# Performance work log

Measured on AMD Instinct MI355X. Metric: run time of the kernel, lower is better.

Reference implementation:

```python
import jax, jax.numpy as jnp
import numpy as np

N = 100000
E = 800000
F_IN = 64
HID = 128


def setup_inputs() -> dict:
    key = jax.random.key(0)
    ks = jax.random.split(key, 10)
    x = jax.random.normal(ks[0], (N, F_IN), dtype=jnp.float32)
    edge_index = jax.random.randint(ks[1], (2, E), 0, N, dtype=jnp.int64)
    s = 0.05
    # PyG GraphConv: lin_rel (with bias) applied to aggregated neighbors, lin_root (no bias) to self
    return {
        "x": x,
        "edge_index": edge_index,
        "W1_rel": jax.random.normal(ks[2], (HID, F_IN), dtype=jnp.float32) * s,
        "b1": jnp.zeros((HID,), dtype=jnp.float32),
        "W1_root": jax.random.normal(ks[3], (HID, F_IN), dtype=jnp.float32) * s,
        "W2_rel": jax.random.normal(ks[4], (HID, HID), dtype=jnp.float32) * s,
        "b2": jnp.zeros((HID,), dtype=jnp.float32),
        "W2_root": jax.random.normal(ks[5], (HID, HID), dtype=jnp.float32) * s,
        "W_fc1": jax.random.normal(ks[6], (20, HID), dtype=jnp.float32) * s,
        "b_fc1": jnp.zeros((20,), dtype=jnp.float32),
        "W_fc2": jax.random.normal(ks[7], (1, 20), dtype=jnp.float32) * s,
        "b_fc2": jnp.zeros((1,), dtype=jnp.float32),
    }


def graph_conv(x, edge_index, W_rel, b_rel, W_root):
    # sum-aggregate source features onto destination nodes (PyG GraphConv, aggr='add')
    src, dst = edge_index[0], edge_index[1]
    agg = jax.ops.segment_sum(x[src], dst, num_segments=N)  # [N, F]
    return agg @ W_rel.T + b_rel + x @ W_root.T


def reference(x, edge_index, W1_rel, b1, W1_root, W2_rel, b2, W2_root,
              W_fc1, b_fc1, W_fc2, b_fc2):
    h = graph_conv(x, edge_index, W1_rel, b1, W1_root)
    h = jax.nn.elu(h)
    h = graph_conv(h, edge_index, W2_rel, b2, W2_root)
    h = jax.nn.relu(h @ W_fc1.T + b_fc1)
    out = h @ W_fc2.T + b_fc2  # [N, 1]
    return out
```

## Files before the change

### kernel.cpp

```cpp
#include <hip/hip_runtime.h>

#define N_NODES 100000
#define N_EDGES 800000
#define FIN 64
#define HID 128
#define NB1 391
#define SRCS_CAP (N_EDGES + 3 * N_NODES)

typedef unsigned short ushort_t;
typedef __attribute__((ext_vector_type(8))) short short8;
typedef __attribute__((ext_vector_type(16))) float fx16;
typedef __attribute__((ext_vector_type(4))) unsigned short us4;

__device__ inline ushort_t f2bf(float f) {
    unsigned u = __float_as_uint(f);
    u += 0x7fffu + ((u >> 16) & 1u);
    return (ushort_t)(u >> 16);
}
__device__ inline float bf2f(ushort_t h) { return __uint_as_float(((unsigned)h) << 16); }

__device__ inline void upadd(float* acc, uint4 A) {
    acc[0] += __uint_as_float(A.x << 16);
    acc[1] += __uint_as_float(A.x & 0xffff0000u);
    acc[2] += __uint_as_float(A.y << 16);
    acc[3] += __uint_as_float(A.y & 0xffff0000u);
    acc[4] += __uint_as_float(A.z << 16);
    acc[5] += __uint_as_float(A.z & 0xffff0000u);
    acc[6] += __uint_as_float(A.w << 16);
    acc[7] += __uint_as_float(A.w & 0xffff0000u);
}

__global__ void zero_int_kernel(int* __restrict__ deg, int* __restrict__ flag,
                                int* __restrict__ srcs) {
    int i = blockIdx.x * 256 + threadIdx.x;
    if (i < N_NODES) deg[i] = 0;
    if (i == 0) *flag = 0;
    for (int k = i; k < SRCS_CAP; k += NB1 * 256) srcs[k] = N_NODES;
}

__global__ void detect_kernel(const int* __restrict__ w, int* __restrict__ flag) {
    int i = blockIdx.x * 256 + threadIdx.x;
    if (i < 8192) {
        if (w[2 * i + 1] != 0) atomicOr(flag, 1);
    }
}

__global__ void hist_kernel(const int* __restrict__ w, const int* __restrict__ flag,
                            int* __restrict__ deg, int* __restrict__ rank) {
    int e = blockIdx.x * 256 + threadIdx.x;
    if (e >= N_EDGES) return;
    int is32 = *flag;
    int d = is32 ? w[N_EDGES + e] : w[2 * (N_EDGES + e)];
    rank[e] = atomicAdd(&deg[d], 1);
}

__global__ void scan1_kernel(const int* __restrict__ deg, int* __restrict__ off,
                             int* __restrict__ bsums) {
    __shared__ int s[256];
    int t = threadIdx.x;
    int i = blockIdx.x * 256 + t;
    int v = (i < N_NODES) ? ((deg[i] + 3) & ~3) : 0;
    s[t] = v;
    __syncthreads();
    for (int d = 1; d < 256; d <<= 1) {
        int w = (t >= d) ? s[t - d] : 0;
        __syncthreads();
        s[t] += w;
        __syncthreads();
    }
    if (i < N_NODES) off[i] = s[t] - v;
    if (t == 255) bsums[blockIdx.x] = s[255];
}

__global__ void scan2_kernel(int* __restrict__ bsums) {
    __shared__ int s[512];
    int t = threadIdx.x;
    int v = (t < NB1) ? bsums[t] : 0;
    s[t] = v;
    __syncthreads();
    for (int d = 1; d < 512; d <<= 1) {
        int w = (t >= d) ? s[t - d] : 0;
        __syncthreads();
        s[t] += w;
        __syncthreads();
    }
    if (t < NB1) bsums[t] = s[t] - v;
    if (t == NB1 - 1) bsums[NB1] = s[t];
}

__global__ void scan3_kernel(int* __restrict__ off, const int* __restrict__ bsums) {
    int i = blockIdx.x * 256 + threadIdx.x;
    if (i < N_NODES) off[i] = off[i] + bsums[blockIdx.x];
    if (i == 0) off[N_NODES] = bsums[NB1];
}

__global__ void scatter_kernel(const int* __restrict__ w, const int* __restrict__ flag,
                               const int* __restrict__ off, const int* __restrict__ rank,
                               int* __restrict__ srcs) {
    int e = blockIdx.x * 256 + threadIdx.x;
    if (e >= N_EDGES) return;
    int is32 = *flag;
    int s = is32 ? w[e] : w[2 * e];
    int d = is32 ? w[N_EDGES + e] : w[2 * (N_EDGES + e)];
    srcs[off[d] + rank[e]] = s;
}

__global__ void cvt_kernel(const float* __restrict__ x, ushort_t* __restrict__ xb,
                           const float* __restrict__ W1rel, const float* __restrict__ W1root,
                           const float* __restrict__ W2rel, const float* __restrict__ W2root,
                           ushort_t* __restrict__ Wb1, ushort_t* __restrict__ Wb2,
                           ushort_t* __restrict__ h1b) {
    int i = blockIdx.x * 256 + threadIdx.x;
    if (i < N_NODES * FIN / 4) {
        float4 v = ((const float4*)x)[i];
        us4 o = {f2bf(v.x), f2bf(v.y), f2bf(v.z), f2bf(v.w)};
        ((us4*)xb)[i] = o;
    }
    us4 z = {0, 0, 0, 0};
    if (i < 16) ((us4*)xb)[(size_t)N_NODES * 16 + i] = z;
    if (i >= 16 && i < 48) ((us4*)h1b)[(size_t)N_NODES * 32 + (i - 16)] = z;
    if (i < HID * HID) {
        int n = i >> 7, k = i & 127;
        float v = (k < FIN) ? W1rel[n * FIN + k] : W1root[n * FIN + (k - FIN)];
        Wb1[i] = f2bf(v);
    }
    if (i < HID * 2 * HID) {
        int n = i >> 8, k = i & 255;
        float v = (k < HID) ? W2rel[n * HID + k] : W2root[n * HID + (k - HID)];
        Wb2[i] = f2bf(v);
    }
}

__global__ void agg1_kernel(const ushort_t* __restrict__ xb, const int* __restrict__ off,
                            const int* __restrict__ srcs, ushort_t* __restrict__ aggb) {
    int wid = (blockIdx.x * 256 + threadIdx.x) >> 6;
    int lane = threadIdx.x & 63;
    int n = lane >> 3;
    unsigned c = lane & 7;
    int node = wid * 8 + n;
    int b = off[node], e = off[node + 1];
    float acc[8];
#pragma unroll
    for (int j = 0; j < 8; j++) acc[j] = 0.f;
    const uint4* rows = (const uint4*)xb;
    for (int p = b; p < e; p += 4) {
        int4 s = *(const int4*)(srcs + p);
        uint4 A = rows[(unsigned)s.x * 8u + c];
        uint4 B = rows[(unsigned)s.y * 8u + c];
        uint4 C = rows[(unsigned)s.z * 8u + c];
        uint4 D = rows[(unsigned)s.w * 8u + c];
        upadd(acc, A);
        upadd(acc, B);
        upadd(acc, C);
        upadd(acc, D);
    }
    uint4 o = {(unsigned)f2bf(acc[0]) | ((unsigned)f2bf(acc[1]) << 16),
               (unsigned)f2bf(acc[2]) | ((unsigned)f2bf(acc[3]) << 16),
               (unsigned)f2bf(acc[4]) | ((unsigned)f2bf(acc[5]) << 16),
               (unsigned)f2bf(acc[6]) | ((unsigned)f2bf(acc[7]) << 16)};
    ((uint4*)(aggb + (size_t)node * FIN))[c] = o;
}

__global__ void agg2_kernel(const ushort_t* __restrict__ h1b, const int* __restrict__ off,
                            const int* __restrict__ srcs, ushort_t* __restrict__ aggb) {
    int wid = (blockIdx.x * 256 + threadIdx.x) >> 6;
    int lane = threadIdx.x & 63;
    int n = lane >> 4;
    unsigned c = lane & 15;
    int node = wid * 4 + n;
    int b = off[node], e = off[node + 1];
    float acc[8];
#pragma unroll
    for (int j = 0; j < 8; j++) acc[j] = 0.f;
    const uint4* rows = (const uint4*)h1b;
    for (int p = b; p < e; p += 4) {
        int4 s = *(const int4*)(srcs + p);
        uint4 A = rows[(unsigned)s.x * 16u + c];
        uint4 B = rows[(unsigned)s.y * 16u + c];
        uint4 C = rows[(unsigned)s.z * 16u + c];
        uint4 D = rows[(unsigned)s.w * 16u + c];
        upadd(acc, A);
        upadd(acc, B);
        upadd(acc, C);
        upadd(acc, D);
    }
    uint4 o = {(unsigned)f2bf(acc[0]) | ((unsigned)f2bf(acc[1]) << 16),
               (unsigned)f2bf(acc[2]) | ((unsigned)f2bf(acc[3]) << 16),
               (unsigned)f2bf(acc[4]) | ((unsigned)f2bf(acc[5]) << 16),
               (unsigned)f2bf(acc[6]) | ((unsigned)f2bf(acc[7]) << 16)};
    ((uint4*)(aggb + (size_t)node * HID))[c] = o;
}

__global__ __launch_bounds__(256) void g1_kernel(
    const ushort_t* __restrict__ aggb, const ushort_t* __restrict__ xb,
    const ushort_t* __restrict__ Wb1, const float* __restrict__ b1,
    ushort_t* __restrict__ h1b) {
    __shared__ short8 wl8[2048];
    ushort_t* wl = (ushort_t*)wl8;
#pragma unroll
    for (int it = 0; it < 8; it++) {
        int q = it * 256 + threadIdx.x;
        int n = q >> 4, c = q & 15;
        short8 v = ((const short8*)Wb1)[q];
        *(short8*)(wl + n * HID + ((c ^ (n & 7)) << 3)) = v;
    }
    __syncthreads();

    int wave = threadIdx.x >> 6;
    int lane = threadIdx.x & 63;
    int nb = blockIdx.x * 128 + wave * 32;
    if (nb >= N_NODES) return;
    int half = lane >> 5, col = lane & 31;
    int nA = nb + col;
    if (nA >= N_NODES) nA = N_NODES - 1;

    short8 areg[8];
#pragma unroll
    for (int s = 0; s < 4; s++)
        areg[s] = *(const short8*)(aggb + (size_t)nA * FIN + s * 16 + half * 8);
#pragma unroll
    for (int s = 4; s < 8; s++)
        areg[s] = *(const short8*)(xb + (size_t)nA * FIN + (s - 4) * 16 + half * 8);

    fx16 acc[4];
#pragma unroll
    for (int jt = 0; jt < 4; jt++)
#pragma unroll
        for (int r = 0; r < 16; r++) acc[jt][r] = 0.f;

#pragma unroll
    for (int s = 0; s < 8; s++) {
        int c = 2 * s + half;
#pragma unroll
        for (int jt = 0; jt < 4; jt++) {
            int n = jt * 32 + col;
            short8 bq = *(const short8*)(wl + n * HID + ((c ^ (n & 7)) << 3));
            acc[jt] = __builtin_amdgcn_mfma_f32_32x32x16_bf16(areg[s], bq, acc[jt], 0, 0, 0);
        }
    }
#pragma unroll
    for (int jt = 0; jt < 4; jt++) {
        int j = jt * 32 + col;
        float bias = b1[j];
#pragma unroll
        for (int r = 0; r < 16; r++) {
            int node = nb + (r & 3) + 8 * (r >> 2) + 4 * half;
            if (node < N_NODES) {
                float v = acc[jt][r] + bias;
                v = v > 0.f ? v : __expf(v) - 1.f;
                h1b[(size_t)node * HID + j] = f2bf(v);
            }
        }
    }
}

__global__ __launch_bounds__(256) void g2h_kernel(
    const ushort_t* __restrict__ agg2b, const ushort_t* __restrict__ h1b,
    const ushort_t* __restrict__ Wb2, const float* __restrict__ b2,
    const float* __restrict__ Wfc1, const float* __restrict__ bfc1,
    const float* __restrict__ Wfc2, const float* __restrict__ bfc2,
    float* __restrict__ out) {
    __shared__ ushort_t smem[21504];
    ushort_t* wl = smem;
    ushort_t* wf = smem + 17408;

#pragma unroll
    for (int it = 0; it < 16; it++) {
        int idx = it * 256 + threadIdx.x;
        int m = idx >> 7, k = idx & 127;
        float v = (m < 20) ? Wfc1[m * HID + k] : 0.f;
        wf[m * 128 + (((k >> 3) ^ (m & 7)) << 3) + (k & 7)] = f2bf(v);
    }
#pragma unroll
    for (int it = 0; it < 8; it++) {
        int q = it * 256 + threadIdx.x;
        int n = q >> 4, c = q & 15;
        short8 v = *(const short8*)(Wb2 + (size_t)n * 256 + c * 8);
        *(short8*)(wl + n * 128 + ((c ^ (n & 7)) << 3)) = v;
    }

    int wave = threadIdx.x >> 6;
    int lane = threadIdx.x & 63;
    int half = lane >> 5, col = lane & 31;
    int nb = blockIdx.x * 128 + wave * 32;
    int nA = nb + col;
    if (nA >= N_NODES) nA = N_NODES - 1;

    short8 areg[16];
#pragma unroll
    for (int s = 0; s < 8; s++)
        areg[s] = *(const short8*)(agg2b + (size_t)nA * HID + s * 16 + half * 8);
#pragma unroll
    for (int s = 8; s < 16; s++)
        areg[s] = *(const short8*)(h1b + (size_t)nA * HID + (s - 8) * 16 + half * 8);

    fx16 acc[4];
#pragma unroll
    for (int jt = 0; jt < 4; jt++)
#pragma unroll
        for (int r = 0; r < 16; r++) acc[jt][r] = 0.f;

    __syncthreads();
#pragma unroll
    for (int s = 0; s < 8; s++) {
        int c = 2 * s + half;
#pragma unroll
        for (int jt = 0; jt < 4; jt++) {
            int n = jt * 32 + col;
            short8 bq = *(const short8*)(wl + n * 128 + ((c ^ (n & 7)) << 3));
            acc[jt] = __builtin_amdgcn_mfma_f32_32x32x16_bf16(areg[s], bq, acc[jt], 0, 0, 0);
        }
    }
    __syncthreads();
#pragma unroll
    for (int it = 0; it < 8; it++) {
        int q = it * 256 + threadIdx.x;
        int n = q >> 4, c = q & 15;
        short8 v = *(const short8*)(Wb2 + (size_t)n * 256 + 128 + c * 8);
        *(short8*)(wl + n * 128 + ((c ^ (n & 7)) << 3)) = v;
    }
    __syncthreads();
#pragma unroll
    for (int s = 8; s < 16; s++) {
        int c = 2 * (s - 8) + half;
#pragma unroll
        for (int jt = 0; jt < 4; jt++) {
            int n = jt * 32 + col;
            short8 bq = *(const short8*)(wl + n * 128 + ((c ^ (n & 7)) << 3));
            acc[jt] = __builtin_amdgcn_mfma_f32_32x32x16_bf16(areg[s], bq, acc[jt], 0, 0, 0);
        }
    }
    __syncthreads();

    ushort_t* tl = smem;
#pragma unroll
    for (int jt = 0; jt < 4; jt++) {
        int j = jt * 32 + col;
        float bias = b2[j];
#pragma unroll
        for (int r = 0; r < 16; r++) {
            int nl = wave * 32 + (r & 3) + 8 * (r >> 2) + 4 * half;
            tl[nl * 136 + j] = f2bf(acc[jt][r] + bias);
        }
    }
    __syncthreads();

    short8 af[8];
#pragma unroll
    for (int s = 0; s < 8; s++)
        af[s] = *(const short8*)(tl + (wave * 32 + col) * 136 + s * 16 + half * 8);
    fx16 fa;
#pragma unroll
    for (int r = 0; r < 16; r++) fa[r] = 0.f;
#pragma unroll
    for (int s = 0; s < 8; s++) {
        int c = 2 * s + half;
        short8 bw = *(const short8*)(wf + col * 128 + ((c ^ (col & 7)) << 3));
        fa = __builtin_amdgcn_mfma_f32_32x32x16_bf16(af[s], bw, fa, 0, 0, 0);
    }
    float biasv = (col < 20) ? bfc1[col] : 0.f;
    float w2v = (col < 20) ? Wfc2[col] : 0.f;
    float bz = bfc2[0];
    float red[16];
#pragma unroll
    for (int r = 0; r < 16; r++) {
        float v = fa[r] + biasv;
        v = (v > 0.f ? v : 0.f) * w2v;
        v += __shfl_xor(v, 1);
        v += __shfl_xor(v, 2);
        v += __shfl_xor(v, 4);
        v += __shfl_xor(v, 8);
        v += __shfl_xor(v, 16);
        red[r] = v;
    }
    if (col == 0) {
#pragma unroll
        for (int r = 0; r < 16; r++) {
            int nl = wave * 32 + (r & 3) + 8 * (r >> 2) + 4 * half;
            int ng = blockIdx.x * 128 + nl;
            if (ng < N_NODES) out[ng] = red[r] + bz;
        }
    }
}

extern "C" void kernel_launch(void* const* d_in, const int* in_sizes, int n_in,
                              void* d_out, int out_size, void* d_ws, size_t ws_size,
                              hipStream_t stream) {
    const float* x = (const float*)d_in[0];
    const int* ei = (const int*)d_in[1];
    const float* W1rel = (const float*)d_in[2];
    const float* b1 = (const float*)d_in[3];
    const float* W1root = (const float*)d_in[4];
    const float* W2rel = (const float*)d_in[5];
    const float* b2 = (const float*)d_in[6];
    const float* W2root = (const float*)d_in[7];
    const float* Wfc1 = (const float*)d_in[8];
    const float* bfc1 = (const float*)d_in[9];
    const float* Wfc2 = (const float*)d_in[10];
    const float* bfc2 = (const float*)d_in[11];
    float* out = (float*)d_out;

    char* ws = (char*)d_ws;
    size_t o = 0;
    auto alloc = [&](size_t bytes) {
        char* p = ws + o;
        o += (bytes + 255) & ~(size_t)255;
        return p;
    };
    int* deg = (int*)alloc((size_t)N_NODES * 4);
    int* off = (int*)alloc((size_t)(N_NODES + 1) * 4);
    int* bsums = (int*)alloc(4096);
    int* flag = (int*)alloc(256);
    int* rank = (int*)alloc((size_t)N_EDGES * 4);
    int* srcs = (int*)alloc((size_t)SRCS_CAP * 4);
    ushort_t* xb = (ushort_t*)alloc((size_t)(N_NODES + 1) * FIN * 2);
    ushort_t* agg1b = (ushort_t*)alloc((size_t)N_NODES * FIN * 2);
    ushort_t* h1b = (ushort_t*)alloc((size_t)(N_NODES + 1) * HID * 2);
    ushort_t* agg2b = (ushort_t*)alloc((size_t)N_NODES * HID * 2);
    ushort_t* Wb1 = (ushort_t*)alloc((size_t)HID * HID * 2);
    ushort_t* Wb2 = (ushort_t*)alloc((size_t)HID * 2 * HID * 2);

    const int GW = (N_NODES + 127) / 128;
    const int GA1 = N_NODES / 32;
    const int GA2 = N_NODES / 16;

    zero_int_kernel<<<NB1, 256, 0, stream>>>(deg, flag, srcs);
    detect_kernel<<<32, 256, 0, stream>>>(ei, flag);
    hist_kernel<<<(N_EDGES + 255) / 256, 256, 0, stream>>>(ei, flag, deg, rank);
    scan1_kernel<<<NB1, 256, 0, stream>>>(deg, off, bsums);
    scan2_kernel<<<1, 512, 0, stream>>>(bsums);
    scan3_kernel<<<NB1, 256, 0, stream>>>(off, bsums);
    scatter_kernel<<<(N_EDGES + 255) / 256, 256, 0, stream>>>(ei, flag, off, rank, srcs);
    cvt_kernel<<<(N_NODES * FIN / 4 + 255) / 256, 256, 0, stream>>>(
        x, xb, W1rel, W1root, W2rel, W2root, Wb1, Wb2, h1b);
    agg1_kernel<<<GA1, 256, 0, stream>>>(xb, off, srcs, agg1b);
    g1_kernel<<<GW, 256, 0, stream>>>(agg1b, xb, Wb1, b1, h1b);
    agg2_kernel<<<GA2, 256, 0, stream>>>(h1b, off, srcs, agg2b);
    g2h_kernel<<<GW, 256, 0, stream>>>(agg2b, h1b, Wb2, b2, Wfc1, bfc1, Wfc2, bfc2, out);
}
```

Baseline: 251.9 us.

## Fuse CSR build and conversion kernels into one cooperative kernel with grid syncs

Replaces eight small launches (zeroing, format detection, histogram, three-phase scan, scatter, bf16 conversion) with a single cooperative kernel of 391 blocks that separates the phases with grid.sync. This removes per-launch overhead and the gaps between dependent tiny kernels. In exchange, the grid-stride loops run with far fewer threads than the original per-edge grids, and the kernel now depends on all 391 blocks being co-resident for the cooperative launch.

```diff
diff --git a/kernel.cpp b/kernel.cpp
--- a/kernel.cpp
+++ b/kernel.cpp
@@ -1,10 +1,14 @@
 #include <hip/hip_runtime.h>
+#include <hip/hip_cooperative_groups.h>
+
+namespace cg = cooperative_groups;
 
 #define N_NODES 100000
 #define N_EDGES 800000
 #define FIN 64
 #define HID 128
 #define NB1 391
+#define GT (NB1 * 256)
 #define SRCS_CAP (N_EDGES + 3 * N_NODES)
 
 typedef unsigned short ushort_t;
@@ -17,7 +21,6 @@
     u += 0x7fffu + ((u >> 16) & 1u);
     return (ushort_t)(u >> 16);
 }
-__device__ inline float bf2f(ushort_t h) { return __uint_as_float(((unsigned)h) << 16); }
 
 __device__ inline void upadd(float* acc, uint4 A) {
     acc[0] += __uint_as_float(A.x << 16);
@@ -30,104 +33,107 @@
     acc[7] += __uint_as_float(A.w & 0xffff0000u);
 }
 
-__global__ void zero_int_kernel(int* __restrict__ deg, int* __restrict__ flag,
-                                int* __restrict__ srcs) {
-    int i = blockIdx.x * 256 + threadIdx.x;
-    if (i < N_NODES) deg[i] = 0;
-    if (i == 0) *flag = 0;
-    for (int k = i; k < SRCS_CAP; k += NB1 * 256) srcs[k] = N_NODES;
-}
-
-__global__ void detect_kernel(const int* __restrict__ w, int* __restrict__ flag) {
-    int i = blockIdx.x * 256 + threadIdx.x;
-    if (i < 8192) {
-        if (w[2 * i + 1] != 0) atomicOr(flag, 1);
-    }
-}
-
-__global__ void hist_kernel(const int* __restrict__ w, const int* __restrict__ flag,
-                            int* __restrict__ deg, int* __restrict__ rank) {
-    int e = blockIdx.x * 256 + threadIdx.x;
-    if (e >= N_EDGES) return;
-    int is32 = *flag;
-    int d = is32 ? w[N_EDGES + e] : w[2 * (N_EDGES + e)];
-    rank[e] = atomicAdd(&deg[d], 1);
-}
-
-__global__ void scan1_kernel(const int* __restrict__ deg, int* __restrict__ off,
-                             int* __restrict__ bsums) {
-    __shared__ int s[256];
-    int t = threadIdx.x;
-    int i = blockIdx.x * 256 + t;
-    int v = (i < N_NODES) ? ((deg[i] + 3) & ~3) : 0;
-    s[t] = v;
-    __syncthreads();
-    for (int d = 1; d < 256; d <<= 1) {
-        int w = (t >= d) ? s[t - d] : 0;
-        __syncthreads();
-        s[t] += w;
-        __syncthreads();
-    }
-    if (i < N_NODES) off[i] = s[t] - v;
-    if (t == 255) bsums[blockIdx.x] = s[255];
-}
-
-__global__ void scan2_kernel(int* __restrict__ bsums) {
+__global__ void __launch_bounds__(256) csr_kernel(
+    const int* __restrict__ ei, const float* __restrict__ x,
+    const float* __restrict__ W1rel, const float* __restrict__ W1root,
+    const float* __restrict__ W2rel, const float* __restrict__ W2root,
+    int* __restrict__ deg, int* __restrict__ flag, int* __restrict__ srcs,
+    int* __restrict__ rank, int* __restrict__ off, int* __restrict__ bsums,
+    ushort_t* __restrict__ xb, ushort_t* __restrict__ h1b,
+    ushort_t* __restrict__ Wb1, ushort_t* __restrict__ Wb2) {
+    cg::grid_group grid = cg::this_grid();
     __shared__ int s[512];
     int t = threadIdx.x;
-    int v = (t < NB1) ? bsums[t] : 0;
-    s[t] = v;
-    __syncthreads();
-    for (int d = 1; d < 512; d <<= 1) {
-        int w = (t >= d) ? s[t - d] : 0;
-        __syncthreads();
-        s[t] += w;
-        __syncthreads();
-    }
-    if (t < NB1) bsums[t] = s[t] - v;
-    if (t == NB1 - 1) bsums[NB1] = s[t];
-}
-
-__global__ void scan3_kernel(int* __restrict__ off, const int* __restrict__ bsums) {
-    int i = blockIdx.x * 256 + threadIdx.x;
-    if (i < N_NODES) off[i] = off[i] + bsums[blockIdx.x];
-    if (i == 0) off[N_NODES] = bsums[NB1];
-}
-
-__global__ void scatter_kernel(const int* __restrict__ w, const int* __restrict__ flag,
-                               const int* __restrict__ off, const int* __restrict__ rank,
-                               int* __restrict__ srcs) {
-    int e = blockIdx.x * 256 + threadIdx.x;
-    if (e >= N_EDGES) return;
-    int is32 = *flag;
-    int s = is32 ? w[e] : w[2 * e];
-    int d = is32 ? w[N_EDGES + e] : w[2 * (N_EDGES + e)];
-    srcs[off[d] + rank[e]] = s;
-}
-
-__global__ void cvt_kernel(const float* __restrict__ x, ushort_t* __restrict__ xb,
-                           const float* __restrict__ W1rel, const float* __restrict__ W1root,
-                           const float* __restrict__ W2rel, const float* __restrict__ W2root,
-                           ushort_t* __restrict__ Wb1, ushort_t* __restrict__ Wb2,
-                           ushort_t* __restrict__ h1b) {
-    int i = blockIdx.x * 256 + threadIdx.x;
-    if (i < N_NODES * FIN / 4) {
+    int gtid = blockIdx.x * 256 + t;
+
+    if (gtid < N_NODES) deg[gtid] = 0;
+    for (int k = gtid; k < SRCS_CAP; k += GT) srcs[k] = N_NODES;
+    for (int i = gtid; i < N_NODES * FIN / 4; i += GT) {
         float4 v = ((const float4*)x)[i];
         us4 o = {f2bf(v.x), f2bf(v.y), f2bf(v.z), f2bf(v.w)};
         ((us4*)xb)[i] = o;
     }
     us4 z = {0, 0, 0, 0};
-    if (i < 16) ((us4*)xb)[(size_t)N_NODES * 16 + i] = z;
-    if (i >= 16 && i < 48) ((us4*)h1b)[(size_t)N_NODES * 32 + (i - 16)] = z;
-    if (i < HID * HID) {
-        int n = i >> 7, k = i & 127;
+    if (gtid < 16) ((us4*)xb)[(size_t)N_NODES * 16 + gtid] = z;
+    if (gtid >= 16 && gtid < 48) ((us4*)h1b)[(size_t)N_NODES * 32 + (gtid - 16)] = z;
+    if (gtid < HID * HID) {
+        int n = gtid >> 7, k = gtid & 127;
         float v = (k < FIN) ? W1rel[n * FIN + k] : W1root[n * FIN + (k - FIN)];
-        Wb1[i] = f2bf(v);
-    }
-    if (i < HID * 2 * HID) {
-        int n = i >> 8, k = i & 255;
+        Wb1[gtid] = f2bf(v);
+    }
+    if (gtid < HID * 2 * HID) {
+        int n = gtid >> 8, k = gtid & 255;
         float v = (k < HID) ? W2rel[n * HID + k] : W2root[n * HID + (k - HID)];
-        Wb2[i] = f2bf(v);
+        Wb2[gtid] = f2bf(v);
+    }
+    if (blockIdx.x == 0) {
+        int bad = 0;
+        for (int i = t; i < 8192; i += 256) bad |= ei[2 * i + 1];
+        s[t] = bad;
+        __syncthreads();
+        for (int d = 128; d > 0; d >>= 1) {
+            if (t < d) s[t] |= s[t + d];
+            __syncthreads();
+        }
+        if (t == 0) *flag = (s[0] != 0) ? 1 : 0;
+        __syncthreads();
+    }
+    __threadfence();
+    grid.sync();
+
+    int is32 = *flag;
+    for (int e = gtid; e < N_EDGES; e += GT) {
+        int d = is32 ? ei[N_EDGES + e] : ei[2 * (N_EDGES + e)];
+        rank[e] = atomicAdd(&deg[d], 1);
+    }
+    __threadfence();
+    grid.sync();
+
+    {
+        int v = (gtid < N_NODES) ? ((deg[gtid] + 3) & ~3) : 0;
+        s[t] = v;
+        __syncthreads();
+        for (int d = 1; d < 256; d <<= 1) {
+            int w = (t >= d) ? s[t - d] : 0;
+            __syncthreads();
+            s[t] += w;
+            __syncthreads();
+        }
+        if (gtid < N_NODES) off[gtid] = s[t] - v;
+        if (t == 255) bsums[blockIdx.x] = s[255];
+    }
+    __threadfence();
+    grid.sync();
+
+    if (blockIdx.x == 0) {
+        int v0 = (2 * t < NB1) ? bsums[2 * t] : 0;
+        int v1 = (2 * t + 1 < NB1) ? bsums[2 * t + 1] : 0;
+        int pair = v0 + v1;
+        s[t] = pair;
+        __syncthreads();
+        for (int d = 1; d < 256; d <<= 1) {
+            int w = (t >= d) ? s[t - d] : 0;
+            __syncthreads();
+            s[t] += w;
+            __syncthreads();
+        }
+        int ex = s[t] - pair;
+        if (2 * t < NB1) bsums[2 * t] = ex;
+        if (2 * t + 1 < NB1) bsums[2 * t + 1] = ex + v0;
+        if (t == 255) bsums[NB1] = s[255];
+    }
+    __threadfence();
+    grid.sync();
+
+    if (gtid < N_NODES) off[gtid] = off[gtid] + bsums[blockIdx.x];
+    if (gtid == 0) off[N_NODES] = bsums[NB1];
+    __threadfence();
+    grid.sync();
+
+    for (int e = gtid; e < N_EDGES; e += GT) {
+        int sv = is32 ? ei[e] : ei[2 * e];
+        int d = is32 ? ei[N_EDGES + e] : ei[2 * (N_EDGES + e)];
+        srcs[off[d] + rank[e]] = sv;
     }
 }
 
@@ -386,8 +392,8 @@
 extern "C" void kernel_launch(void* const* d_in, const int* in_sizes, int n_in,
                               void* d_out, int out_size, void* d_ws, size_t ws_size,
                               hipStream_t stream) {
+    const int* ei = (const int*)d_in[1];
     const float* x = (const float*)d_in[0];
-    const int* ei = (const int*)d_in[1];
     const float* W1rel = (const float*)d_in[2];
     const float* b1 = (const float*)d_in[3];
     const float* W1root = (const float*)d_in[4];
@@ -424,15 +430,12 @@
     const int GA1 = N_NODES / 32;
     const int GA2 = N_NODES / 16;
 
-    zero_int_kernel<<<NB1, 256, 0, stream>>>(deg, flag, srcs);
-    detect_kernel<<<32, 256, 0, stream>>>(ei, flag);
-    hist_kernel<<<(N_EDGES + 255) / 256, 256, 0, stream>>>(ei, flag, deg, rank);
-    scan1_kernel<<<NB1, 256, 0, stream>>>(deg, off, bsums);
-    scan2_kernel<<<1, 512, 0, stream>>>(bsums);
-    scan3_kernel<<<NB1, 256, 0, stream>>>(off, bsums);
-    scatter_kernel<<<(N_EDGES + 255) / 256, 256, 0, stream>>>(ei, flag, off, rank, srcs);
-    cvt_kernel<<<(N_NODES * FIN / 4 + 255) / 256, 256, 0, stream>>>(
-        x, xb, W1rel, W1root, W2rel, W2root, Wb1, Wb2, h1b);
+    void* args[] = {(void*)&ei, (void*)&x, (void*)&W1rel, (void*)&W1root,
+                    (void*)&W2rel, (void*)&W2root,
+                    (void*)&deg, (void*)&flag, (void*)&srcs, (void*)&rank,
+                    (void*)&off, (void*)&bsums,
+                    (void*)&xb, (void*)&h1b, (void*)&Wb1, (void*)&Wb2};
+    hipLaunchCooperativeKernel((void*)csr_kernel, dim3(NB1), dim3(256), args, 0, stream);
     agg1_kernel<<<GA1, 256, 0, stream>>>(xb, off, srcs, agg1b);
     g1_kernel<<<GW, 256, 0, stream>>>(agg1b, xb, Wb1, b1, h1b);
     agg2_kernel<<<GA2, 256, 0, stream>>>(h1b, off, srcs, agg2b);
```

Measured after the change: 654.1 us. 160% more time.
